# Kernel optimization log

Hardware: AMD Instinct MI355X
Metric: run time of the kernel (lower is better)

Reference implementation:

```python
import jax, jax.numpy as jnp
import numpy as np

A2B = 1.8897259886          # angstrom -> bohr
EV2HA = 0.0367493
NUM_RBF = 16
R_MIN = 0.5 * A2B
R_MAX = 4.0 * A2B           # r_max_angstroms=4.0 from gnn_config
RBF_WIDTH = (R_MAX - R_MIN) / NUM_RBF
N_NODES = 100_000
N_EDGES = 3_200_000
EMBED_DIM = 16
N_ELEMS = 4
CODES_PER_ELEM = 4          # all elements are core -> max_codes_per_element
TOTAL_CODES = N_ELEMS * CODES_PER_ELEM
NUM_PAIRS = 10
CODE_OWNER = np.repeat(np.arange(N_ELEMS), CODES_PER_ELEM)  # element owning each code


def setup_inputs() -> dict:
    key = jax.random.key(0)
    ks = jax.random.split(key, 12)
    N, E, D = N_NODES, N_EDGES, EMBED_DIM
    inv_sp = lambda v: np.float32(np.log(np.expm1(v)))  # inverse_softplus
    return {
        "elem_idx": jax.random.randint(ks[0], (N,), 0, N_ELEMS),
        "edge_index": jax.random.randint(ks[1], (2, E), 0, N),
        "distances": jax.random.uniform(ks[2], (E,), minval=1.0, maxval=7.5),  # bohr
        "pair_idx": jax.random.randint(ks[3], (E,), 0, NUM_PAIRS),
        "embed": jax.random.normal(ks[4], (N_ELEMS, D)),
        "fw1": jax.random.normal(ks[5], (D, NUM_RBF)) * 0.3,
        "fb1": jnp.zeros((D,)),
        "fw2": jax.random.normal(ks[6], (D, D)) * 0.3,
        "fb2": jnp.zeros((D,)),
        "mw1": jax.random.normal(ks[7], (D, D)) * 0.3,
        "mb1": jnp.zeros((D,)),
        "mw2": jax.random.normal(ks[8], (3, D)) * 0.05,  # zero-init in orig; small random for a live baseline
        "mb2": jnp.zeros((3,)),
        "codebook": jax.random.normal(ks[9], (TOTAL_CODES, D)),
        "raw_D_e": jnp.full((NUM_PAIRS,), inv_sp(0.1 * EV2HA)),
        "raw_alpha": jnp.full((NUM_PAIRS,), inv_sp(1.5 / A2B)),
        "raw_r0": jnp.full((NUM_PAIRS,), np.float32(3.0 * A2B)),
    }


def reference(elem_idx, edge_index, distances, pair_idx, embed,
              fw1, fb1, fw2, fb2, mw1, mb1, mw2, mb2,
              codebook, raw_D_e, raw_alpha, raw_r0):
    # --- EnvironmentEncoder: gather + edge filter + scatter_add ---
    h = embed[elem_idx]                                              # [N, D]
    centers = jnp.linspace(R_MIN, R_MAX, NUM_RBF, dtype=distances.dtype)
    rbf = jnp.exp(-0.5 * ((distances[:, None] - centers) / RBF_WIDTH) ** 2)  # [E, RBF]
    W = jax.nn.silu(rbf @ fw1.T + fb1) @ fw2.T + fb2                 # [E, D]
    src, tgt = edge_index[0], edge_index[1]
    messages = h[tgt] * W                                            # [E, D]
    agg = jax.ops.segment_sum(messages, src, num_segments=h.shape[0])
    h = h + agg                                                      # [N, D]

    # --- VectorQuantizer (eval path): per-element masked cdist + argmin ---
    d2 = (jnp.sum(h * h, axis=1, keepdims=True)
          - 2.0 * h @ codebook.T
          + jnp.sum(codebook * codebook, axis=1))                    # [N, C] squared dist
    owner = jnp.asarray(CODE_OWNER)
    valid = elem_idx[:, None] == owner[None, :]                      # [N, C]
    atom_types = jnp.argmin(jnp.where(valid, d2, jnp.inf), axis=1)   # [N]
    z_q = codebook[atom_types]                                       # [N, D]
    h_q = h + jax.lax.stop_gradient(z_q - h)                         # straight-through
    # all elements have >1 code -> commitment over all atoms
    vq_loss = 0.25 * jnp.mean((h - jax.lax.stop_gradient(z_q)) ** 2)

    # --- MorseParameterPredictor: edge gather + MLP ---
    pair_feat = h_q[src] + h_q[tgt]                                  # [E, D]
    delta = jax.nn.silu(pair_feat @ mw1.T + mb1) @ mw2.T + mb2       # [E, 3]

    D_e = jax.nn.softplus(raw_D_e[pair_idx] + delta[:, 0])
    alpha = jax.nn.softplus(raw_alpha[pair_idx] + delta[:, 1])
    r0 = raw_r0[pair_idx] + delta[:, 2]
    params = jnp.stack([D_e, alpha, r0], axis=-1)                    # [E, 3]
    return params, vq_loss
```

## Files before the change

kernel.cpp:

```cpp
#include <hip/hip_runtime.h>
#include <stdint.h>

#define A2B   1.8897259886f
#define R_MIN (0.5f * A2B)
#define R_MAX (4.0f * A2B)

#define EPB   2048
#define CSH   9
#define QSCALE 1048576.0f
#define QINV   (1.0f / 1048576.0f)

__global__ void __launch_bounds__(256) k_bucket(
        const int* __restrict__ src, const int* __restrict__ tgt,
        const int* __restrict__ elem, const float* __restrict__ dist,
        const float* __restrict__ fw1, float* __restrict__ fw1t,
        int* __restrict__ gCursor, float* __restrict__ dBuf,
        unsigned short* __restrict__ kBuf, int CAP, int E)
{
    __shared__ int cnt[4][256];
    __shared__ int lbase[256], gbase[256];
    __shared__ int wofs[4][256];
    __shared__ int sd[256];
    __shared__ float ldsD[EPB];
    __shared__ unsigned short ldsK[EPB];
    __shared__ unsigned char ldsB[EPB];
    int t = threadIdx.x;
    int w = t >> 6;
    if (blockIdx.x == 0)
        fw1t[t] = fw1[(t & 15) * 16 + (t >> 4)];
    cnt[0][t] = 0; cnt[1][t] = 0; cnt[2][t] = 0; cnt[3][t] = 0;
    __syncthreads();
    int e0 = blockIdx.x * EPB;
    int eEnd = (e0 + EPB < E) ? e0 + EPB : E;
    int nloc = eEnd - e0;

    float dv[8]; int bv[8]; unsigned short kv[8];
    #pragma unroll
    for (int j = 0; j < 8; ++j) {
        int e = e0 + t + j * 256;
        if (e < eEnd) {
            int s = src[e];
            int q = elem[tgt[e]];
            dv[j] = dist[e];
            int b = s >> CSH;
            bv[j] = b;
            kv[j] = (unsigned short)(((s - (b << CSH)) << 2) | q);
            atomicAdd(&cnt[w][b], 1);
        }
    }
    __syncthreads();
    {
        int c0 = cnt[0][t], c1 = cnt[1][t], c2 = cnt[2][t], c3 = cnt[3][t];
        int tot = c0 + c1 + c2 + c3;
        sd[t] = tot;
        __syncthreads();
        #pragma unroll
        for (int o = 1; o < 256; o <<= 1) {
            int x = (t >= o) ? sd[t - o] : 0;
            __syncthreads();
            sd[t] += x;
            __syncthreads();
        }
        int lb = sd[t] - tot;
        lbase[t] = lb;
        gbase[t] = (tot > 0) ? atomicAdd(&gCursor[t], tot) : 0;
        wofs[0][t] = lb;
        wofs[1][t] = lb + c0;
        wofs[2][t] = lb + c0 + c1;
        wofs[3][t] = lb + c0 + c1 + c2;
        cnt[0][t] = 0; cnt[1][t] = 0; cnt[2][t] = 0; cnt[3][t] = 0;
    }
    __syncthreads();
    #pragma unroll
    for (int j = 0; j < 8; ++j) {
        int e = e0 + t + j * 256;
        if (e < eEnd) {
            int b = bv[j];
            int pos = wofs[w][b] + atomicAdd(&cnt[w][b], 1);
            ldsD[pos] = dv[j];
            ldsK[pos] = kv[j];
            ldsB[pos] = (unsigned char)b;
        }
    }
    __syncthreads();
    for (int j = t; j < nloc; j += 256) {
        int b = (int)ldsB[j];
        int din = gbase[b] + (j - lbase[b]);
        if (din < CAP) {
            size_t idx = (size_t)b * CAP + din;
            dBuf[idx] = ldsD[j];
            kBuf[idx] = ldsK[j];
        }
    }
}

__global__ void __launch_bounds__(256) k_bin(
        const float* __restrict__ dBuf, const unsigned short* __restrict__ kBuf,
        const int* __restrict__ gCursor, int* __restrict__ offs,
        float* __restrict__ payload, int CAP, int NBUK, int N, int E)
{
    __shared__ int lcnt[512];
    __shared__ int sd[256];
    __shared__ int s_base;
    int t = threadIdx.x;
    int cb = blockIdx.x >> 1, fc = blockIdx.x & 1;
    lcnt[t] = 0; lcnt[t + 256] = 0;
    int v = (t < NBUK) ? gCursor[t] : 0;
    sd[t] = v; __syncthreads();
    #pragma unroll
    for (int o = 1; o < 256; o <<= 1) {
        int x = (t >= o) ? sd[t - o] : 0;
        __syncthreads();
        sd[t] += x;
        __syncthreads();
    }
    if (t == cb) s_base = sd[t] - v;
    __syncthreads();
    int base = s_base;

    int n0 = cb << CSH;
    int n1 = n0 + (1 << CSH); if (n1 > N) n1 = N;
    int m  = n1 - n0;
    int cntE = gCursor[cb]; if (cntE > CAP) cntE = CAP;
    if (cb == 0 && fc == 0 && t == 0) offs[N] = E;

    const float* dB = dBuf + (size_t)cb * CAP;
    const unsigned short* kB = kBuf + (size_t)cb * CAP;
    for (int i = t; i < cntE; i += 256)
        atomicAdd(&lcnt[kB[i] >> 2], 1);
    __syncthreads();
    int b2 = t * 2;
    int v0 = (b2 < m)     ? lcnt[b2]     : 0;
    int v1 = (b2 + 1 < m) ? lcnt[b2 + 1] : 0;
    int tsum = v0 + v1;
    sd[t] = tsum; __syncthreads();
    #pragma unroll
    for (int o = 1; o < 256; o <<= 1) {
        int x = (t >= o) ? sd[t - o] : 0;
        __syncthreads();
        sd[t] += x;
        __syncthreads();
    }
    int run = sd[t] - tsum;
    if (b2 < m) {
        if ((b2 >> 8) == fc) offs[n0 + b2] = base + run;
        lcnt[b2] = run; run += v0;
    }
    if (b2 + 1 < m) {
        if (((b2 + 1) >> 8) == fc) offs[n0 + b2 + 1] = base + run;
        lcnt[b2 + 1] = run;
    }
    __syncthreads();
    for (int i = t; i < cntE; i += 256) {
        int kv = kB[i];
        int l = kv >> 2;
        if ((l >> 8) == fc) {
            int pos = atomicAdd(&lcnt[l], 1);
            unsigned db = __float_as_uint(dB[i]);
            payload[base + pos] = __uint_as_float((db & ~3u) | (unsigned)(kv & 3));
        }
    }
}

__global__ void __launch_bounds__(256) k_gather(
        const int* __restrict__ elem, const float* __restrict__ embed,
        const float* __restrict__ codebook,
        const float4* __restrict__ fw1t4, const float* __restrict__ fb1,
        const float* __restrict__ fw2, const float* __restrict__ fb2,
        const int* __restrict__ offs, const float* __restrict__ payload,
        int* __restrict__ atype, float* __restrict__ loss, int N)
{
    __shared__ float4 s_fw2v[64];
    __shared__ float s_cb[256];
    __shared__ float s_fb1[16], s_fb2[16], s_emb[64], s_cbn[16];
    __shared__ float s_red[4];
    __shared__ int s_ord[64];
    int t = threadIdx.x;
    {
        float* f2 = (float*)s_fw2v;
        f2[t] = fw2[t];
        s_cb[t] = codebook[t];
    }
    if (t < 16) { s_fb1[t] = fb1[t]; s_fb2[t] = fb2[t]; }
    if (t < 64) s_emb[t] = embed[t];
    int nbase = blockIdx.x * 64;
    if (t < 64) {
        int n = nbase + t;
        int dg = (n < N) ? (offs[n + 1] - offs[n]) : 0x7FFF;
        s_ord[t] = (dg << 6) | t;
    }
    __syncthreads();
    if (t < 16) {
        float s = 0.f;
        #pragma unroll
        for (int j = 0; j < 16; ++j) { float c = s_cb[t * 16 + j]; s += c * c; }
        s_cbn[t] = s;
    }
    for (int ksz = 2; ksz <= 64; ksz <<= 1) {
        for (int jj = ksz >> 1; jj > 0; jj >>= 1) {
            __syncthreads();
            if (t < 64) {
                int ixj = t ^ jj;
                if (ixj > t) {
                    int a = s_ord[t], b = s_ord[ixj];
                    bool asc = ((t & ksz) == 0);
                    if (asc ? (a > b) : (a < b)) { s_ord[t] = b; s_ord[ixj] = a; }
                }
            }
        }
    }
    __syncthreads();

    int node = nbase + (s_ord[t >> 2] & 63);
    int sub  = t & 3;
    float lp = 0.0f;
    if (node < N) {
        int o0 = offs[node], o1 = offs[node + 1];
        int G0[16], G1[16], G2[16], G3[16];
        #pragma unroll
        for (int j = 0; j < 16; ++j) { G0[j]=0; G1[j]=0; G2[j]=0; G3[j]=0; }
        int c0 = 0, c1 = 0, c2 = 0, c3 = 0;

        const float invw   = 16.0f / (R_MAX - R_MIN);
        const float u0base = R_MIN * invw;
        const float kstep  = 16.0f / 15.0f;
        for (int i = o0 + sub; i < o1; i += 8) {
            int ii = i + 4;
            bool has2 = (ii < o1);
            unsigned p0 = __float_as_uint(payload[i]);
            unsigned p1 = has2 ? __float_as_uint(payload[ii]) : p0;
            int q0 = (int)(p0 & 3u), q1 = (int)(p1 & 3u);
            float d0 = __uint_as_float(p0 & ~3u);
            float d1 = __uint_as_float(p1 & ~3u);
            float ua = d0 * invw - u0base;
            float ub = d1 * invw - u0base;
            float g0[16], g1[16];
            #pragma unroll
            for (int i2 = 0; i2 < 16; ++i2) { g0[i2] = s_fb1[i2]; g1[i2] = s_fb1[i2]; }
            #pragma clang loop unroll(disable)
            for (int k = 0; k < 16; ++k) {
                float r0 = __expf(-0.5f * ua * ua);
                float r1 = __expf(-0.5f * ub * ub);
                float4 w0 = fw1t4[k*4+0], w1 = fw1t4[k*4+1];
                float4 w2 = fw1t4[k*4+2], w3 = fw1t4[k*4+3];
                g0[0]+=r0*w0.x;  g0[1]+=r0*w0.y;  g0[2]+=r0*w0.z;  g0[3]+=r0*w0.w;
                g0[4]+=r0*w1.x;  g0[5]+=r0*w1.y;  g0[6]+=r0*w1.z;  g0[7]+=r0*w1.w;
                g0[8]+=r0*w2.x;  g0[9]+=r0*w2.y;  g0[10]+=r0*w2.z; g0[11]+=r0*w2.w;
                g0[12]+=r0*w3.x; g0[13]+=r0*w3.y; g0[14]+=r0*w3.z; g0[15]+=r0*w3.w;
                g1[0]+=r1*w0.x;  g1[1]+=r1*w0.y;  g1[2]+=r1*w0.z;  g1[3]+=r1*w0.w;
                g1[4]+=r1*w1.x;  g1[5]+=r1*w1.y;  g1[6]+=r1*w1.z;  g1[7]+=r1*w1.w;
                g1[8]+=r1*w2.x;  g1[9]+=r1*w2.y;  g1[10]+=r1*w2.z; g1[11]+=r1*w2.w;
                g1[12]+=r1*w3.x; g1[13]+=r1*w3.y; g1[14]+=r1*w3.z; g1[15]+=r1*w3.w;
                ua -= kstep; ub -= kstep;
            }
            {
                c0 += (q0==0); c1 += (q0==1); c2 += (q0==2); c3 += (q0==3);
                #pragma unroll
                for (int i2 = 0; i2 < 16; ++i2) {
                    float a = g0[i2];
                    float s = a * __builtin_amdgcn_rcpf(1.0f + __expf(-a));
                    int sq = __float2int_rn(s * QSCALE);
                    G0[i2] += (q0==0) ? sq : 0;
                    G1[i2] += (q0==1) ? sq : 0;
                    G2[i2] += (q0==2) ? sq : 0;
                    G3[i2] += (q0==3) ? sq : 0;
                }
            }
            if (has2) {
                c0 += (q1==0); c1 += (q1==1); c2 += (q1==2); c3 += (q1==3);
                #pragma unroll
                for (int i2 = 0; i2 < 16; ++i2) {
                    float a = g1[i2];
                    float s = a * __builtin_amdgcn_rcpf(1.0f + __expf(-a));
                    int sq = __float2int_rn(s * QSCALE);
                    G0[i2] += (q1==0) ? sq : 0;
                    G1[i2] += (q1==1) ? sq : 0;
                    G2[i2] += (q1==2) ? sq : 0;
                    G3[i2] += (q1==3) ? sq : 0;
                }
            }
        }
        #pragma unroll
        for (int mm = 1; mm <= 2; mm <<= 1) {
            #pragma unroll
            for (int j = 0; j < 16; ++j) {
                G0[j] += __shfl_xor(G0[j], mm, 64);
                G1[j] += __shfl_xor(G1[j], mm, 64);
                G2[j] += __shfl_xor(G2[j], mm, 64);
                G3[j] += __shfl_xor(G3[j], mm, 64);
            }
            c0 += __shfl_xor(c0, mm, 64);
            c1 += __shfl_xor(c1, mm, 64);
            c2 += __shfl_xor(c2, mm, 64);
            c3 += __shfl_xor(c3, mm, 64);
        }
        float Gs[16];
        #pragma unroll
        for (int j = 0; j < 16; ++j) {
            int gq = (sub==0) ? G0[j] : (sub==1) ? G1[j] : (sub==2) ? G2[j] : G3[j];
            Gs[j] = (float)gq * QINV;
        }
        float cs = (float)((sub==0) ? c0 : (sub==1) ? c1 : (sub==2) ? c2 : c3);
        const float* er = s_emb + sub * 16;
        float acc[16];
        #pragma clang loop unroll_count(4)
        for (int j = 0; j < 16; ++j) {
            float4 f0 = s_fw2v[j*4+0], f1 = s_fw2v[j*4+1];
            float4 f2 = s_fw2v[j*4+2], f3 = s_fw2v[j*4+3];
            float w = Gs[0]*f0.x  + Gs[1]*f0.y  + Gs[2]*f0.z  + Gs[3]*f0.w
                    + Gs[4]*f1.x  + Gs[5]*f1.y  + Gs[6]*f1.z  + Gs[7]*f1.w
                    + Gs[8]*f2.x  + Gs[9]*f2.y  + Gs[10]*f2.z + Gs[11]*f2.w
                    + Gs[12]*f3.x + Gs[13]*f3.y + Gs[14]*f3.z + Gs[15]*f3.w;
            acc[j] = (w + cs * s_fb2[j]) * er[j];
        }
        #pragma unroll
        for (int mm = 1; mm <= 2; mm <<= 1) {
            #pragma unroll
            for (int j = 0; j < 16; ++j)
                acc[j] += __shfl_xor(acc[j], mm, 64);
        }
        int qn = elem[node];
        float h[16], hh = 0.f;
        #pragma unroll
        for (int j = 0; j < 16; ++j) {
            h[j] = acc[j] + s_emb[qn * 16 + j];
            hh += h[j] * h[j];
        }
        float best = __builtin_inff(); int bi = 0;
        #pragma unroll
        for (int c = 0; c < 4; ++c) {
            int code = qn * 4 + c;
            float dot = 0.f;
            #pragma unroll
            for (int j = 0; j < 16; ++j) dot += h[j] * s_cb[code * 16 + j];
            float d2 = hh - 2.0f * dot + s_cbn[code];
            if (d2 < best) { best = d2; bi = code; }
        }
        if (sub == 0) {
            atype[node] = bi;
            #pragma unroll
            for (int j = 0; j < 16; ++j) {
                float df = h[j] - s_cb[bi * 16 + j];
                lp += df * df;
            }
        }
    }
    #pragma unroll
    for (int o = 32; o > 0; o >>= 1) lp += __shfl_down(lp, o, 64);
    int wid = t >> 6;
    if ((t & 63) == 0) s_red[wid] = lp;
    __syncthreads();
    if (t == 0) atomicAdd(loss, s_red[0] + s_red[1] + s_red[2] + s_red[3]);
}

__global__ void __launch_bounds__(256) k_table(
        const float* __restrict__ codebook,
        const float* __restrict__ mw1, const float* __restrict__ mb1,
        const float* __restrict__ mw2, const float* __restrict__ mb2,
        const float* __restrict__ rD, const float* __restrict__ rA,
        const float* __restrict__ rR,
        const float* __restrict__ loss, float4* __restrict__ table,
        float* __restrict__ out_loss, float inv_nd)
{
    __shared__ float s_cb[256], s_mw1[256], s_mb1[16], s_mw2[48], s_mb2[3];
    __shared__ float s_rd[10], s_ra[10], s_rr[10];
    int tid = threadIdx.x;
    s_cb[tid] = codebook[tid];
    s_mw1[tid] = mw1[tid];
    if (tid < 16) s_mb1[tid] = mb1[tid];
    if (tid < 48) s_mw2[tid] = mw2[tid];
    if (tid < 3)  s_mb2[tid] = mb2[tid];
    if (tid < 10) { s_rd[tid] = rD[tid]; s_ra[tid] = rA[tid]; s_rr[tid] = rR[tid]; }
    __syncthreads();

    int a = tid >> 4, b = tid & 15;
    float pf[16];
    #pragma unroll
    for (int j = 0; j < 16; ++j) pf[j] = s_cb[a * 16 + j] + s_cb[b * 16 + j];
    float hid[16];
    #pragma unroll
    for (int i = 0; i < 16; ++i) {
        float acc = s_mb1[i];
        #pragma unroll
        for (int j = 0; j < 16; ++j) acc += pf[j] * s_mw1[i * 16 + j];
        hid[i] = acc / (1.0f + __expf(-acc));
    }
    float del[3];
    #pragma unroll
    for (int r = 0; r < 3; ++r) {
        float acc = s_mb2[r];
        #pragma unroll
        for (int i = 0; i < 16; ++i) acc += hid[i] * s_mw2[r * 16 + i];
        del[r] = acc;
    }
    #pragma unroll
    for (int p = 0; p < 10; ++p) {
        float xd = s_rd[p] + del[0];
        float xa = s_ra[p] + del[1];
        float De = (xd > 20.f) ? xd : log1pf(__expf(xd));
        float al = (xa > 20.f) ? xa : log1pf(__expf(xa));
        float r0 = s_rr[p] + del[2];
        table[tid * 10 + p] = make_float4(De, al, r0, 0.f);
    }
    if (tid == 0) out_loss[0] = 0.25f * loss[0] * inv_nd;
}

__global__ void __launch_bounds__(256) k_out(
        const int* __restrict__ src, const int* __restrict__ tgt,
        const int* __restrict__ pidx, const int* __restrict__ atype,
        const float4* __restrict__ table, float2* __restrict__ out, int Ehalf)
{
    int i = blockIdx.x * 256 + threadIdx.x;
    if (i >= Ehalf) return;
    int2 s2 = ((const int2*)src)[i];
    int2 t2 = ((const int2*)tgt)[i];
    int2 p2 = ((const int2*)pidx)[i];
    int i0 = (atype[s2.x] * 16 + atype[t2.x]) * 10 + p2.x;
    int i1 = (atype[s2.y] * 16 + atype[t2.y]) * 10 + p2.y;
    float4 t0 = table[i0];
    float4 t1 = table[i1];
    float2* op = out + (size_t)3 * i;
    op[0] = make_float2(t0.x, t0.y);
    op[1] = make_float2(t0.z, t1.x);
    op[2] = make_float2(t1.y, t1.z);
}

extern "C" void kernel_launch(void* const* d_in, const int* in_sizes, int n_in,
                              void* d_out, int out_size, void* d_ws, size_t ws_size,
                              hipStream_t stream)
{
    (void)n_in;
    const int*   elem  = (const int*)d_in[0];
    const int*   eidx  = (const int*)d_in[1];
    const float* dist  = (const float*)d_in[2];
    const int*   pidx  = (const int*)d_in[3];
    const float* embed = (const float*)d_in[4];
    const float* fw1   = (const float*)d_in[5];
    const float* fb1   = (const float*)d_in[6];
    const float* fw2   = (const float*)d_in[7];
    const float* fb2   = (const float*)d_in[8];
    const float* mw1   = (const float*)d_in[9];
    const float* mb1   = (const float*)d_in[10];
    const float* mw2   = (const float*)d_in[11];
    const float* mb2   = (const float*)d_in[12];
    const float* cb    = (const float*)d_in[13];
    const float* rD    = (const float*)d_in[14];
    const float* rA    = (const float*)d_in[15];
    const float* rR    = (const float*)d_in[16];

    int N = in_sizes[0];
    int E = in_sizes[2];
    const int* src = eidx;
    const int* tgt = eidx + E;

    int NBUK = (N + (1 << CSH) - 1) >> CSH;
    if (NBUK > 256) return;
    long long expv = ((long long)E << CSH) / N;
    int CAP = (int)(expv + expv / 16 + 256);

    size_t outBytes = (size_t)out_size * 4;
    char* ob = (char*)d_out;
    size_t oc = 0;
    float* dBuf = (float*)(ob + oc);           oc += (size_t)NBUK * CAP * 4;
    unsigned short* kBuf = (unsigned short*)(ob + oc); oc += (size_t)NBUK * CAP * 2;
    oc = (oc + 3) & ~(size_t)3;
    float* payload = (float*)(ob + oc);        oc += (size_t)E * 4;
    int*   offs    = (int*)(ob + oc);          oc += (size_t)(N + 1) * 4;
    if (oc > outBytes) return;

    char* ws = (char*)d_ws;
    size_t cur = 0;
    int*   gCursor = (int*)(ws + cur);  cur += 256 * 4;
    float* loss    = (float*)(ws + cur); cur += 4;
    size_t clearB = cur;
    cur = (cur + 15) & ~(size_t)15;
    float* fw1t    = (float*)(ws + cur); cur += 256 * 4;
    int*   atype   = (int*)(ws + cur);  cur += (size_t)N * 4;
    cur = (cur + 15) & ~(size_t)15;
    float4* table  = (float4*)(ws + cur); cur += 2560 * sizeof(float4);
    if (ws_size < cur) return;

    hipMemsetAsync(d_ws, 0, clearB, stream);

    k_bucket<<<(E + EPB - 1) / EPB, 256, 0, stream>>>(
        src, tgt, elem, dist, fw1, fw1t, gCursor, dBuf, kBuf, CAP, E);
    k_bin<<<NBUK * 2, 256, 0, stream>>>(dBuf, kBuf, gCursor, offs, payload,
                                        CAP, NBUK, N, E);
    k_gather<<<(N + 63) / 64, 256, 0, stream>>>(elem, embed, cb,
                                                (const float4*)fw1t, fb1,
                                                fw2, fb2, offs, payload,
                                                atype, loss, N);
    float* outl = (float*)d_out + (size_t)3 * E;
    k_table<<<1, 256, 0, stream>>>(cb, mw1, mb1, mw2, mb2, rD, rA, rR,
                                   loss, table, outl,
                                   1.0f / (float)((size_t)N * 16));
    k_out<<<(E / 2 + 255) / 256, 256, 0, stream>>>(src, tgt, pidx, atype, table,
                                                   (float2*)d_out, E / 2);
}
```

Measured before the change: 266.4 us.

## Halve bucket width to 256 nodes and drop dual-pass binning blocks

Bucket size shrinks from 512 to 256 source nodes, doubling the bucket count (up to 512). The first-pass kernel now handles two buckets per thread in its scan. The binning kernel runs one block per bucket instead of two half-blocks that each rescanned the whole bucket, so duplicated reads of the bucket data are removed. Capacity slack rises to 1/8 to absorb higher variance in the smaller buckets, at the cost of more LDS in the bucketing kernel and more scattered global writes per block.

Result: no change. 265.5 us (-0.3%).

```diff
diff --git a/kernel.cpp b/kernel.cpp
--- a/kernel.cpp
+++ b/kernel.cpp
@@ -6,7 +6,8 @@
 #define R_MAX (4.0f * A2B)
 
 #define EPB   2048
-#define CSH   9
+#define CSH   8
+#define NBMAX 512
 #define QSCALE 1048576.0f
 #define QINV   (1.0f / 1048576.0f)
 
@@ -15,20 +16,24 @@
         const int* __restrict__ elem, const float* __restrict__ dist,
         const float* __restrict__ fw1, float* __restrict__ fw1t,
         int* __restrict__ gCursor, float* __restrict__ dBuf,
-        unsigned short* __restrict__ kBuf, int CAP, int E)
+        unsigned short* __restrict__ kBuf, int CAP, int NBUK, int E)
 {
-    __shared__ int cnt[4][256];
-    __shared__ int lbase[256], gbase[256];
-    __shared__ int wofs[4][256];
+    __shared__ int cnt[4][NBMAX];
+    __shared__ int lbase[NBMAX], gbase[NBMAX];
+    __shared__ int wofs[4][NBMAX];
     __shared__ int sd[256];
     __shared__ float ldsD[EPB];
     __shared__ unsigned short ldsK[EPB];
-    __shared__ unsigned char ldsB[EPB];
+    __shared__ short ldsB[EPB];
     int t = threadIdx.x;
     int w = t >> 6;
     if (blockIdx.x == 0)
         fw1t[t] = fw1[(t & 15) * 16 + (t >> 4)];
-    cnt[0][t] = 0; cnt[1][t] = 0; cnt[2][t] = 0; cnt[3][t] = 0;
+    {
+        int i0 = t * 2, i1 = t * 2 + 1;
+        cnt[0][i0]=0; cnt[1][i0]=0; cnt[2][i0]=0; cnt[3][i0]=0;
+        cnt[0][i1]=0; cnt[1][i1]=0; cnt[2][i1]=0; cnt[3][i1]=0;
+    }
     __syncthreads();
     int e0 = blockIdx.x * EPB;
     int eEnd = (e0 + EPB < E) ? e0 + EPB : E;
@@ -50,9 +55,12 @@
     }
     __syncthreads();
     {
-        int c0 = cnt[0][t], c1 = cnt[1][t], c2 = cnt[2][t], c3 = cnt[3][t];
-        int tot = c0 + c1 + c2 + c3;
-        sd[t] = tot;
+        int bA = t * 2, bB = t * 2 + 1;
+        int a0=cnt[0][bA], a1=cnt[1][bA], a2=cnt[2][bA], a3=cnt[3][bA];
+        int b0=cnt[0][bB], b1=cnt[1][bB], b2=cnt[2][bB], b3=cnt[3][bB];
+        int totA = a0+a1+a2+a3, totB = b0+b1+b2+b3;
+        int tsum = totA + totB;
+        sd[t] = tsum;
         __syncthreads();
         #pragma unroll
         for (int o = 1; o < 256; o <<= 1) {
@@ -61,14 +69,17 @@
             sd[t] += x;
             __syncthreads();
         }
-        int lb = sd[t] - tot;
-        lbase[t] = lb;
-        gbase[t] = (tot > 0) ? atomicAdd(&gCursor[t], tot) : 0;
-        wofs[0][t] = lb;
-        wofs[1][t] = lb + c0;
-        wofs[2][t] = lb + c0 + c1;
-        wofs[3][t] = lb + c0 + c1 + c2;
-        cnt[0][t] = 0; cnt[1][t] = 0; cnt[2][t] = 0; cnt[3][t] = 0;
+        int lbA = sd[t] - tsum;
+        int lbB = lbA + totA;
+        lbase[bA] = lbA; lbase[bB] = lbB;
+        gbase[bA] = (totA > 0) ? atomicAdd(&gCursor[bA], totA) : 0;
+        gbase[bB] = (totB > 0) ? atomicAdd(&gCursor[bB], totB) : 0;
+        wofs[0][bA] = lbA;          wofs[1][bA] = lbA + a0;
+        wofs[2][bA] = lbA + a0+a1;  wofs[3][bA] = lbA + a0+a1+a2;
+        wofs[0][bB] = lbB;          wofs[1][bB] = lbB + b0;
+        wofs[2][bB] = lbB + b0+b1;  wofs[3][bB] = lbB + b0+b1+b2;
+        cnt[0][bA]=0; cnt[1][bA]=0; cnt[2][bA]=0; cnt[3][bA]=0;
+        cnt[0][bB]=0; cnt[1][bB]=0; cnt[2][bB]=0; cnt[3][bB]=0;
     }
     __syncthreads();
     #pragma unroll
@@ -79,7 +90,7 @@
             int pos = wofs[w][b] + atomicAdd(&cnt[w][b], 1);
             ldsD[pos] = dv[j];
             ldsK[pos] = kv[j];
-            ldsB[pos] = (unsigned char)b;
+            ldsB[pos] = (short)b;
         }
     }
     __syncthreads();
@@ -99,14 +110,17 @@
         const int* __restrict__ gCursor, int* __restrict__ offs,
         float* __restrict__ payload, int CAP, int NBUK, int N, int E)
 {
-    __shared__ int lcnt[512];
+    __shared__ int lcnt[256];
     __shared__ int sd[256];
     __shared__ int s_base;
     int t = threadIdx.x;
-    int cb = blockIdx.x >> 1, fc = blockIdx.x & 1;
-    lcnt[t] = 0; lcnt[t + 256] = 0;
-    int v = (t < NBUK) ? gCursor[t] : 0;
-    sd[t] = v; __syncthreads();
+    int cb = blockIdx.x;
+    lcnt[t] = 0;
+    int b0 = t * 2, b1 = t * 2 + 1;
+    int v0 = (b0 < NBUK) ? gCursor[b0] : 0;
+    int v1 = (b1 < NBUK) ? gCursor[b1] : 0;
+    int tsum = v0 + v1;
+    sd[t] = tsum; __syncthreads();
     #pragma unroll
     for (int o = 1; o < 256; o <<= 1) {
         int x = (t >= o) ? sd[t - o] : 0;
@@ -114,7 +128,8 @@
         sd[t] += x;
         __syncthreads();
     }
-    if (t == cb) s_base = sd[t] - v;
+    if (b0 == cb) s_base = sd[t] - tsum;
+    if (b1 == cb) s_base = sd[t] - tsum + v0;
     __syncthreads();
     int base = s_base;
 
@@ -122,18 +137,15 @@
     int n1 = n0 + (1 << CSH); if (n1 > N) n1 = N;
     int m  = n1 - n0;
     int cntE = gCursor[cb]; if (cntE > CAP) cntE = CAP;
-    if (cb == 0 && fc == 0 && t == 0) offs[N] = E;
+    if (cb == 0 && t == 0) offs[N] = E;
 
     const float* dB = dBuf + (size_t)cb * CAP;
     const unsigned short* kB = kBuf + (size_t)cb * CAP;
     for (int i = t; i < cntE; i += 256)
         atomicAdd(&lcnt[kB[i] >> 2], 1);
     __syncthreads();
-    int b2 = t * 2;
-    int v0 = (b2 < m)     ? lcnt[b2]     : 0;
-    int v1 = (b2 + 1 < m) ? lcnt[b2 + 1] : 0;
-    int tsum = v0 + v1;
-    sd[t] = tsum; __syncthreads();
+    int v = (t < m) ? lcnt[t] : 0;
+    sd[t] = v; __syncthreads();
     #pragma unroll
     for (int o = 1; o < 256; o <<= 1) {
         int x = (t >= o) ? sd[t - o] : 0;
@@ -141,24 +153,17 @@
         sd[t] += x;
         __syncthreads();
     }
-    int run = sd[t] - tsum;
-    if (b2 < m) {
-        if ((b2 >> 8) == fc) offs[n0 + b2] = base + run;
-        lcnt[b2] = run; run += v0;
-    }
-    if (b2 + 1 < m) {
-        if (((b2 + 1) >> 8) == fc) offs[n0 + b2 + 1] = base + run;
-        lcnt[b2 + 1] = run;
-    }
+    int ex = sd[t] - v;
+    if (t < m) offs[n0 + t] = base + ex;
+    __syncthreads();
+    if (t < m) lcnt[t] = ex;
     __syncthreads();
     for (int i = t; i < cntE; i += 256) {
         int kv = kB[i];
         int l = kv >> 2;
-        if ((l >> 8) == fc) {
-            int pos = atomicAdd(&lcnt[l], 1);
-            unsigned db = __float_as_uint(dB[i]);
-            payload[base + pos] = __uint_as_float((db & ~3u) | (unsigned)(kv & 3));
-        }
+        int pos = atomicAdd(&lcnt[l], 1);
+        unsigned db = __float_as_uint(dB[i]);
+        payload[base + pos] = __uint_as_float((db & ~3u) | (unsigned)(kv & 3));
     }
 }
 
@@ -454,9 +459,9 @@
     const int* tgt = eidx + E;
 
     int NBUK = (N + (1 << CSH) - 1) >> CSH;
-    if (NBUK > 256) return;
+    if (NBUK > NBMAX) return;
     long long expv = ((long long)E << CSH) / N;
-    int CAP = (int)(expv + expv / 16 + 256);
+    int CAP = (int)(expv + expv / 8 + 256);
 
     size_t outBytes = (size_t)out_size * 4;
     char* ob = (char*)d_out;
@@ -470,7 +475,7 @@
 
     char* ws = (char*)d_ws;
     size_t cur = 0;
-    int*   gCursor = (int*)(ws + cur);  cur += 256 * 4;
+    int*   gCursor = (int*)(ws + cur);  cur += NBMAX * 4;
     float* loss    = (float*)(ws + cur); cur += 4;
     size_t clearB = cur;
     cur = (cur + 15) & ~(size_t)15;
@@ -483,9 +488,9 @@
     hipMemsetAsync(d_ws, 0, clearB, stream);
 
     k_bucket<<<(E + EPB - 1) / EPB, 256, 0, stream>>>(
-        src, tgt, elem, dist, fw1, fw1t, gCursor, dBuf, kBuf, CAP, E);
-    k_bin<<<NBUK * 2, 256, 0, stream>>>(dBuf, kBuf, gCursor, offs, payload,
-                                        CAP, NBUK, N, E);
+        src, tgt, elem, dist, fw1, fw1t, gCursor, dBuf, kBuf, CAP, NBUK, E);
+    k_bin<<<NBUK, 256, 0, stream>>>(dBuf, kBuf, gCursor, offs, payload,
+                                    CAP, NBUK, N, E);
     k_gather<<<(N + 63) / 64, 256, 0, stream>>>(elem, embed, cb,
                                                 (const float4*)fw1t, fb1,
                                                 fw2, fb2, offs, payload,
```
